# Kernel tuning notes

Hardware: AMD Instinct MI355X
Metric: run time of the kernel (lower is better)

Reference implementation:

```python
import jax, jax.numpy as jnp
import numpy as np

B, C, H, W = 4, 512, 64, 64
WS = 32          # window size (square)
NHEADS = 8
GROUPS = 32      # GroupNorm groups (ldm Normalize)
EPS = 1e-6


def setup_inputs() -> dict:
    key = jax.random.key(0)
    ks = jax.random.split(key, 6)
    p = lambda k: jax.random.normal(k, (C, C), jnp.float32) * 0.02
    return {
        "x": jax.random.normal(ks[0], (B, C, H, W), jnp.float32),
        "norm_scale": jnp.ones((C,), jnp.float32),
        "norm_bias": jnp.zeros((C,), jnp.float32),
        "wq": p(ks[1]), "bq": jnp.zeros((C,), jnp.float32),
        "wk": p(ks[2]), "bk": jnp.zeros((C,), jnp.float32),
        "wv": p(ks[3]), "bv": jnp.zeros((C,), jnp.float32),
        "wo": p(ks[4]), "bo": jnp.zeros((C,), jnp.float32),
    }


def _group_norm(x, scale, bias):
    b, c, h, w = x.shape
    xg = x.reshape(b, GROUPS, c // GROUPS, h, w)
    mu = xg.mean(axis=(2, 3, 4), keepdims=True)
    var = ((xg - mu) ** 2).mean(axis=(2, 3, 4), keepdims=True)
    xn = ((xg - mu) * jax.lax.rsqrt(var + EPS)).reshape(b, c, h, w)
    return xn * scale[None, :, None, None] + bias[None, :, None, None]


def _conv1x1(t, w, b):
    return jnp.einsum('bchw,oc->bohw', t, w) + b[None, :, None, None]


def reference(x, norm_scale, norm_bias, wq, bq, wk, bk, wv, bv, wo, bo):
    b, c, hh, ww = x.shape
    h_ = _group_norm(x, norm_scale, norm_bias)

    # window partition: b c (h w1) (w w2) -> (b h w) c w1 w2  (H,W divisible by WS, no pad)
    nH, nW = hh // WS, ww // WS
    h_ = h_.reshape(b, c, nH, WS, nW, WS).transpose(0, 2, 4, 1, 3, 5)
    h_ = h_.reshape(b * nH * nW, c, WS, WS)

    q = _conv1x1(h_, wq, bq)
    k = _conv1x1(h_, wk, bk)
    v = _conv1x1(h_, wv, bv)

    bw = q.shape[0]
    n = WS * WS
    d = c // NHEADS

    def to_heads(t):  # b c h w -> b heads n d
        t = t.reshape(bw, c, n).transpose(0, 2, 1)          # b n c
        return t.reshape(bw, n, NHEADS, d).transpose(0, 2, 1, 3)

    q, k, v = map(to_heads, (q, k, v))

    scale = 1.0 / jnp.sqrt(jnp.asarray(d, q.dtype))
    scores = jnp.einsum('bhnd,bhmd->bhnm', q, k) * scale    # [bw, heads, n, n]
    attn = jax.nn.softmax(scores, axis=-1)
    out = jnp.einsum('bhnm,bhmd->bhnd', attn, v)
    out = out.transpose(0, 2, 1, 3).reshape(bw, n, c)       # b n c

    # window reverse: (b h w) (w1 w2) c -> b c (h w1) (w w2)
    out = out.reshape(b, nH, nW, WS, WS, c).transpose(0, 5, 1, 3, 2, 4)
    out = out.reshape(b, c, hh, ww)

    out = _conv1x1(out, wo, bo)
    return x + out
```

## Files before the change

### kernel.cpp

```cpp
#include <hip/hip_runtime.h>
#include <math.h>

typedef __bf16 bf16_t;
typedef bf16_t bf16x8 __attribute__((ext_vector_type(8)));
typedef float f32x16 __attribute__((ext_vector_type(16)));
typedef unsigned int u32x4 __attribute__((ext_vector_type(4)));

#define MFMA32(a, b, c) __builtin_amdgcn_mfma_f32_32x32x16_bf16(a, b, c, 0, 0, 0)
#define ROWOF(r, h) (((r) & 3) + 8 * ((r) >> 2) + 4 * (h))


static constexpr size_t OFF_STATS = 0;
static constexpr size_t OFF_W     = 4096;
static constexpr size_t OFF_HT    = OFF_W + 4u * 524288u;
static constexpr size_t OFF_Q     = OFF_HT + 16777216u;
static constexpr size_t OFF_K     = OFF_Q + 16777216u;
static constexpr size_t OFF_V     = OFF_K + 16777216u;
static constexpr size_t OFF_O     = OFF_HT;

__device__ __forceinline__ unsigned short f2bf(float f) {
  unsigned int u = __float_as_uint(f);
  u += 0x7fffu + ((u >> 16) & 1u);
  return (unsigned short)(u >> 16);
}

__global__ __launch_bounds__(256) void wconv_k(const float* __restrict__ w0, const float* __restrict__ w1,
                                               const float* __restrict__ w2, const float* __restrict__ w3,
                                               unsigned short* __restrict__ dst) {
  const float* srcs[4] = {w0, w1, w2, w3};
  const float* src = srcs[blockIdx.y];
  unsigned short* d = dst + (size_t)blockIdx.y * 262144u;
  int i = (blockIdx.x * 256 + threadIdx.x) * 4;
  float4 v = *(const float4*)(src + i);
  unsigned int lo = (unsigned int)f2bf(v.x) | ((unsigned int)f2bf(v.y) << 16);
  unsigned int hi = (unsigned int)f2bf(v.z) | ((unsigned int)f2bf(v.w) << 16);
  uint2 pk; pk.x = lo; pk.y = hi;
  *(uint2*)(d + i) = pk;
}

__global__ __launch_bounds__(256) void gn_stats_k(const float* __restrict__ x, float* __restrict__ stats) {
  int bg = blockIdx.x;
  const float* p = x + (size_t)bg * 65536u;
  int t = threadIdx.x;
  float s = 0.f, ss = 0.f;
  for (int i = t * 4; i < 65536; i += 1024) {
    float4 v = *(const float4*)(p + i);
    s += v.x + v.y + v.z + v.w;
    ss += v.x * v.x + v.y * v.y + v.z * v.z + v.w * v.w;
  }
  for (int m = 1; m <= 32; m <<= 1) { s += __shfl_xor(s, m); ss += __shfl_xor(ss, m); }
  __shared__ float rs[4], rss[4];
  int wv = t >> 6;
  if ((t & 63) == 0) { rs[wv] = s; rss[wv] = ss; }
  __syncthreads();
  if (t == 0) {
    s = rs[0] + rs[1] + rs[2] + rs[3];
    ss = rss[0] + rss[1] + rss[2] + rss[3];
    float mean = s * (1.f / 65536.f);
    float var = ss * (1.f / 65536.f) - mean * mean;
    stats[bg * 2] = mean;
    stats[bg * 2 + 1] = rsqrtf(var + 1e-6f);
  }
}

__global__ __launch_bounds__(256) void gn_apply_k(const float* __restrict__ x, const float* __restrict__ scale,
                                                  const float* __restrict__ bias, const float* __restrict__ stats,
                                                  unsigned short* __restrict__ ht) {
  __shared__ float tile[64][65];
  int blk = blockIdx.x;
  int b = blk >> 9, cblk = (blk >> 6) & 7, sblk = blk & 63;
  int c0 = cblk * 64, s0 = sblk * 64;
  int t = threadIdx.x;
#pragma unroll
  for (int p = 0; p < 4; ++p) {
    int i = p * 16 + (t >> 4);
    int j = (t & 15) * 4;
    int c = c0 + i;
    float mean = stats[(b * 32 + (c >> 4)) * 2];
    float rstd = stats[(b * 32 + (c >> 4)) * 2 + 1];
    float a = rstd * scale[c];
    float b2 = bias[c] - mean * a;
    float4 v = *(const float4*)(x + ((size_t)(b * 512 + c)) * 4096u + s0 + j);
    tile[i][j + 0] = v.x * a + b2;
    tile[i][j + 1] = v.y * a + b2;
    tile[i][j + 2] = v.z * a + b2;
    tile[i][j + 3] = v.w * a + b2;
  }
  __syncthreads();
#pragma unroll
  for (int p = 0; p < 8; ++p) {
    int jj = p * 8 + (t >> 5);
    int c2 = (t & 31) * 2;
    unsigned int pk = (unsigned int)f2bf(tile[c2][jj]) | ((unsigned int)f2bf(tile[c2 + 1][jj]) << 16);
    *(unsigned int*)(ht + ((size_t)b * 4096u + s0 + jj) * 512u + c0 + c2) = pk;
  }
}

__global__ __launch_bounds__(256, 2) void qkv_gemm_k(const unsigned short* __restrict__ wbf,
                                                     const unsigned short* __restrict__ ht,
                                                     const float* __restrict__ bq, const float* __restrict__ bk,
                                                     const float* __restrict__ bv,
                                                     unsigned short* __restrict__ Qatt,
                                                     unsigned short* __restrict__ Katt,
                                                     unsigned short* __restrict__ Vt) {
  int proj = blockIdx.z >> 2, b = blockIdx.z & 3;
  const unsigned short* W = wbf + (size_t)proj * 262144u;
  const float* biasp = (proj == 0) ? bq : (proj == 1) ? bk : bv;
  int o0 = blockIdx.x * 128, s0 = blockIdx.y * 128;
  __shared__ unsigned short Wl[128 * 72];
  __shared__ unsigned short Xl[128 * 72];
  int t = threadIdx.x, lane = t & 63, wv = t >> 6;
  int col_l = lane & 31, half = lane >> 5;
  int qm = (wv >> 1) * 64, qn = (wv & 1) * 64;
  f32x16 acc[2][2];
#pragma unroll
  for (int i = 0; i < 2; i++)
#pragma unroll
    for (int j = 0; j < 2; j++)
#pragma unroll
      for (int r = 0; r < 16; r++) acc[i][j][r] = 0.f;

  const unsigned short* hb = ht + ((size_t)b * 4096u + s0) * 512u;
  for (int kb = 0; kb < 512; kb += 64) {
    __syncthreads();
    {
      int row = t >> 3, ch = (t & 7) * 8;
#pragma unroll
      for (int p = 0; p < 4; ++p, row += 32) {
        *(uint4*)(Wl + row * 72 + ch) = *(const uint4*)(W + (size_t)(o0 + row) * 512u + kb + ch);
        *(uint4*)(Xl + row * 72 + ch) = *(const uint4*)(hb + (size_t)row * 512u + kb + ch);
      }
    }
    __syncthreads();
    const unsigned short* aT = (proj == 2) ? Wl : Xl;
    const unsigned short* bT = (proj == 2) ? Xl : Wl;
#pragma unroll
    for (int ks = 0; ks < 64; ks += 16) {
      bf16x8 a0 = *(const bf16x8*)(aT + (qm + col_l) * 72 + ks + 8 * half);
      bf16x8 a1 = *(const bf16x8*)(aT + (qm + 32 + col_l) * 72 + ks + 8 * half);
      bf16x8 b0 = *(const bf16x8*)(bT + (qn + col_l) * 72 + ks + 8 * half);
      bf16x8 b1 = *(const bf16x8*)(bT + (qn + 32 + col_l) * 72 + ks + 8 * half);
      acc[0][0] = MFMA32(a0, b0, acc[0][0]);
      acc[0][1] = MFMA32(a0, b1, acc[0][1]);
      acc[1][0] = MFMA32(a1, b0, acc[1][0]);
      acc[1][1] = MFMA32(a1, b1, acc[1][1]);
    }
  }

  if (proj <= 1) {
    unsigned short* dst = (proj == 0) ? Qatt : Katt;
#pragma unroll
    for (int i = 0; i < 2; i++)
#pragma unroll
      for (int j = 0; j < 2; j++) {
        int o = o0 + qn + 32 * j + col_l;
        int head = o >> 6, dd = o & 63;
        float bb = biasp[o];
#pragma unroll
        for (int r = 0; r < 16; r++) {
          int s = s0 + qm + 32 * i + ROWOF(r, half);
          int h = s >> 6, w = s & 63;
          int win = b * 4 + (h >> 5) * 2 + (w >> 5);
          int n = ((h & 31) << 5) | (w & 31);
          dst[(((size_t)(win * 8 + head)) * 1024u + n) * 64u + dd] = f2bf(acc[i][j][r] + bb);
        }
      }
  } else {
#pragma unroll
    for (int i = 0; i < 2; i++)
#pragma unroll
      for (int j = 0; j < 2; j++) {
        int s = s0 + qn + 32 * j + col_l;
        int h = s >> 6, w = s & 63;
        int win = b * 4 + (h >> 5) * 2 + (w >> 5);
        int n = ((h & 31) << 5) | (w & 31);
#pragma unroll
        for (int r = 0; r < 16; r++) {
          int o = o0 + qm + 32 * i + ROWOF(r, half);
          int head = o >> 6, dd = o & 63;
          Vt[(((size_t)(win * 8 + head)) * 64u + dd) * 1024u + n] = f2bf(acc[i][j][r] + biasp[o]);
        }
      }
  }
}

__global__ __launch_bounds__(256, 3) void attn_k(const unsigned short* __restrict__ Qatt,
                                                 const unsigned short* __restrict__ Katt,
                                                 const unsigned short* __restrict__ Vt,
                                                 unsigned short* __restrict__ Oimg) {
  int wh_idx = blockIdx.x, rb = blockIdx.y;
  int win = wh_idx >> 3, head = wh_idx & 7;
  int t = threadIdx.x, lane = t & 63, wv = t >> 6;
  int col_l = lane & 31, half = lane >> 5;
  __shared__ unsigned short Kl[128 * 72];
  __shared__ unsigned short Vl[64 * 136];
  const size_t wh = (size_t)wh_idx;
  const unsigned short* Qb = Qatt + wh * 65536u;
  const unsigned short* Kb = Katt + wh * 65536u;
  const unsigned short* Vb = Vt + wh * 65536u;

  int qrow = rb * 128 + wv * 32 + col_l;
  bf16x8 qf[4];
#pragma unroll
  for (int kk = 0; kk < 4; kk++) qf[kk] = *(const bf16x8*)(Qb + (size_t)qrow * 64u + kk * 16 + 8 * half);

  f32x16 oacc[2];
#pragma unroll
  for (int j = 0; j < 2; j++)
#pragma unroll
    for (int r = 0; r < 16; r++) oacc[j][r] = 0.f;
  float lsum = 0.f;

  const float SC = 0.125f * 1.44269504f;

  for (int kt = 0; kt < 8; ++kt) {
    __syncthreads();
    {
      int row = t >> 3, ch = (t & 7) * 8;
#pragma unroll
      for (int p = 0; p < 4; ++p, row += 32)
        *(uint4*)(Kl + row * 72 + ch) = *(const uint4*)(Kb + ((size_t)(kt * 128 + row)) * 64u + ch);
      int vrow = t >> 4, vch = (t & 15) * 8;
#pragma unroll
      for (int p = 0; p < 4; ++p, vrow += 16)
        *(uint4*)(Vl + vrow * 136 + vch) = *(const uint4*)(Vb + (size_t)vrow * 1024u + kt * 128 + vch);
    }
    __syncthreads();

    f32x16 sacc[4];
#pragma unroll
    for (int jb = 0; jb < 4; jb++)
#pragma unroll
      for (int r = 0; r < 16; r++) sacc[jb][r] = 0.f;
#pragma unroll
    for (int jb = 0; jb < 4; jb++) {
#pragma unroll
      for (int kk = 0; kk < 4; kk++) {
        bf16x8 af = *(const bf16x8*)(Kl + (jb * 32 + col_l) * 72 + kk * 16 + 8 * half);
        sacc[jb] = MFMA32(af, qf[kk], sacc[jb]);
      }
    }

#pragma unroll
    for (int jb = 0; jb < 4; jb++) {
      float p[16];
#pragma unroll
      for (int r = 0; r < 16; r++) p[r] = __builtin_amdgcn_exp2f(sacc[jb][r] * SC);
      float ps = ((p[0] + p[1]) + (p[2] + p[3])) + ((p[4] + p[5]) + (p[6] + p[7]));
      ps += ((p[8] + p[9]) + (p[10] + p[11])) + ((p[12] + p[13]) + (p[14] + p[15]));
      lsum += ps;
      unsigned int pk[8];
#pragma unroll
      for (int j = 0; j < 8; j++)
        pk[j] = __builtin_amdgcn_perm(__float_as_uint(p[2 * j + 1]), __float_as_uint(p[2 * j]), 0x07060302u);
      unsigned int rA = __shfl_xor((int)(half ? pk[0] : pk[2]), 32);
      unsigned int rB = __shfl_xor((int)(half ? pk[1] : pk[3]), 32);
      unsigned int rC = __shfl_xor((int)(half ? pk[4] : pk[6]), 32);
      unsigned int rD = __shfl_xor((int)(half ? pk[5] : pk[7]), 32);
      u32x4 f0, f1;
      f0[0] = half ? rA : pk[0];
      f0[1] = half ? rB : pk[1];
      f0[2] = half ? pk[2] : rA;
      f0[3] = half ? pk[3] : rB;
      f1[0] = half ? rC : pk[4];
      f1[1] = half ? rD : pk[5];
      f1[2] = half ? pk[6] : rC;
      f1[3] = half ? pk[7] : rD;
      bf16x8 pa0 = __builtin_bit_cast(bf16x8, f0);
      bf16x8 pa1 = __builtin_bit_cast(bf16x8, f1);
#pragma unroll
      for (int dblk = 0; dblk < 2; dblk++) {
        bf16x8 v0 = *(const bf16x8*)(Vl + (dblk * 32 + col_l) * 136 + (jb * 2 + 0) * 16 + 8 * half);
        bf16x8 v1 = *(const bf16x8*)(Vl + (dblk * 32 + col_l) * 136 + (jb * 2 + 1) * 16 + 8 * half);
        oacc[dblk] = MFMA32(pa0, v0, oacc[dblk]);
        oacc[dblk] = MFMA32(pa1, v1, oacc[dblk]);
      }
    }
  }

  float l = lsum + __shfl_xor(lsum, 32);
  float inv = 1.f / l;

  int b = win >> 2, whn = (win >> 1) & 1, wwn = win & 1;
#pragma unroll
  for (int r = 0; r < 16; r++) {
    int qr = ROWOF(r, half);
    float invr = __shfl(inv, qr);
    int ntok = rb * 128 + wv * 32 + qr;
    int h = whn * 32 + (ntok >> 5), w = wwn * 32 + (ntok & 31);
    int s = h * 64 + w;
    size_t rowbase = ((size_t)b * 4096u + s) * 512u + head * 64;
    Oimg[rowbase + col_l] = f2bf(oacc[0][r] * invr);
    Oimg[rowbase + 32 + col_l] = f2bf(oacc[1][r] * invr);
  }
}

__global__ __launch_bounds__(256, 2) void out_gemm_k(const unsigned short* __restrict__ wo_bf,
                                                     const unsigned short* __restrict__ Oimg,
                                                     const float* __restrict__ bo, const float* __restrict__ x,
                                                     float* __restrict__ out) {
  int b = blockIdx.z;
  int o0 = blockIdx.x * 128, s0 = blockIdx.y * 128;
  __shared__ unsigned short Wl[128 * 72];
  __shared__ unsigned short Xl[128 * 72];
  int t = threadIdx.x, lane = t & 63, wv = t >> 6;
  int col_l = lane & 31, half = lane >> 5;
  int qm = (wv >> 1) * 64, qn = (wv & 1) * 64;
  f32x16 acc[2][2];
#pragma unroll
  for (int i = 0; i < 2; i++)
#pragma unroll
    for (int j = 0; j < 2; j++)
#pragma unroll
      for (int r = 0; r < 16; r++) acc[i][j][r] = 0.f;

  const unsigned short* ob = Oimg + ((size_t)b * 4096u + s0) * 512u;
  for (int kb = 0; kb < 512; kb += 64) {
    __syncthreads();
    {
      int row = t >> 3, ch = (t & 7) * 8;
#pragma unroll
      for (int p = 0; p < 4; ++p, row += 32) {
        *(uint4*)(Wl + row * 72 + ch) = *(const uint4*)(wo_bf + (size_t)(o0 + row) * 512u + kb + ch);
        *(uint4*)(Xl + row * 72 + ch) = *(const uint4*)(ob + (size_t)row * 512u + kb + ch);
      }
    }
    __syncthreads();
#pragma unroll
    for (int ks = 0; ks < 64; ks += 16) {
      bf16x8 a0 = *(const bf16x8*)(Wl + (qm + col_l) * 72 + ks + 8 * half);
      bf16x8 a1 = *(const bf16x8*)(Wl + (qm + 32 + col_l) * 72 + ks + 8 * half);
      bf16x8 b0 = *(const bf16x8*)(Xl + (qn + col_l) * 72 + ks + 8 * half);
      bf16x8 b1 = *(const bf16x8*)(Xl + (qn + 32 + col_l) * 72 + ks + 8 * half);
      acc[0][0] = MFMA32(a0, b0, acc[0][0]);
      acc[0][1] = MFMA32(a0, b1, acc[0][1]);
      acc[1][0] = MFMA32(a1, b0, acc[1][0]);
      acc[1][1] = MFMA32(a1, b1, acc[1][1]);
    }
  }
#pragma unroll
  for (int i = 0; i < 2; i++)
#pragma unroll
    for (int j = 0; j < 2; j++) {
      int s = s0 + qn + 32 * j + col_l;
#pragma unroll
      for (int r = 0; r < 16; r++) {
        int o = o0 + qm + 32 * i + ROWOF(r, half);
        size_t idx = ((size_t)b * 512u + o) * 4096u + s;
        out[idx] = x[idx] + acc[i][j][r] + bo[o];
      }
    }
}

extern "C" void kernel_launch(void* const* d_in, const int* in_sizes, int n_in,
                              void* d_out, int out_size, void* d_ws, size_t ws_size,
                              hipStream_t stream) {
  const float* x = (const float*)d_in[0];
  const float* nsc = (const float*)d_in[1];
  const float* nbi = (const float*)d_in[2];
  const float* wq = (const float*)d_in[3];
  const float* bq = (const float*)d_in[4];
  const float* wk = (const float*)d_in[5];
  const float* bk = (const float*)d_in[6];
  const float* wvp = (const float*)d_in[7];
  const float* bv = (const float*)d_in[8];
  const float* wo = (const float*)d_in[9];
  const float* bo = (const float*)d_in[10];
  float* out = (float*)d_out;
  char* ws = (char*)d_ws;

  float* stats = (float*)(ws + OFF_STATS);
  unsigned short* wbf = (unsigned short*)(ws + OFF_W);
  unsigned short* ht = (unsigned short*)(ws + OFF_HT);
  unsigned short* Qatt = (unsigned short*)(ws + OFF_Q);
  unsigned short* Katt = (unsigned short*)(ws + OFF_K);
  unsigned short* Vt = (unsigned short*)(ws + OFF_V);
  unsigned short* Oimg = (unsigned short*)(ws + OFF_O);

  wconv_k<<<dim3(256, 4), 256, 0, stream>>>(wq, wk, wvp, wo, wbf);
  gn_stats_k<<<128, 256, 0, stream>>>(x, stats);
  gn_apply_k<<<2048, 256, 0, stream>>>(x, nsc, nbi, stats, ht);
  qkv_gemm_k<<<dim3(4, 32, 12), 256, 0, stream>>>(wbf, ht, bq, bk, bv, Qatt, Katt, Vt);
  attn_k<<<dim3(128, 8), 256, 0, stream>>>(Qatt, Katt, Vt, Oimg);
  out_gemm_k<<<dim3(4, 32, 4), 256, 0, stream>>>(wbf + 3u * 262144u, Oimg, bo, x, out);
}
```

Measured before the change: 272.7 us.

## Double-buffer shared-memory tiles with register prefetch in GEMM and attention kernels

Converts the QKV GEMM, attention and output GEMM kernels to a double-buffered LDS scheme. The next K-slice (or K/V tile) is loaded from global memory into registers while the MFMAs run on the current buffer, and one of the two barriers per iteration is dropped. In exchange it doubles LDS use and raises register pressure. The attention kernel's launch-bounds occupancy hint is lowered from 3 to 2 blocks per CU to make room.

Result: slower. 325.1 us (+19.2%).

```diff
diff --git a/kernel.cpp b/kernel.cpp
--- a/kernel.cpp
+++ b/kernel.cpp
@@ -107,8 +107,8 @@
   const unsigned short* W = wbf + (size_t)proj * 262144u;
   const float* biasp = (proj == 0) ? bq : (proj == 1) ? bk : bv;
   int o0 = blockIdx.x * 128, s0 = blockIdx.y * 128;
-  __shared__ unsigned short Wl[128 * 72];
-  __shared__ unsigned short Xl[128 * 72];
+  __shared__ unsigned short Wl[2][128 * 72];
+  __shared__ unsigned short Xl[2][128 * 72];
   int t = threadIdx.x, lane = t & 63, wv = t >> 6;
   int col_l = lane & 31, half = lane >> 5;
   int qm = (wv >> 1) * 64, qn = (wv & 1) * 64;
@@ -121,19 +121,35 @@
       for (int r = 0; r < 16; r++) acc[i][j][r] = 0.f;
 
   const unsigned short* hb = ht + ((size_t)b * 4096u + s0) * 512u;
-  for (int kb = 0; kb < 512; kb += 64) {
+  int row = t >> 3, ch = (t & 7) * 8;
+
+  uint4 wr[4], xr[4];
+#pragma unroll
+  for (int p = 0; p < 4; ++p) {
+    wr[p] = *(const uint4*)(W + (size_t)(o0 + row + 32 * p) * 512u + ch);
+    xr[p] = *(const uint4*)(hb + (size_t)(row + 32 * p) * 512u + ch);
+  }
+
+  for (int kb8 = 0; kb8 < 8; ++kb8) {
+    int buf = kb8 & 1;
+    unsigned short* Wc = Wl[buf];
+    unsigned short* Xc = Xl[buf];
+#pragma unroll
+    for (int p = 0; p < 4; ++p) {
+      *(uint4*)(Wc + (row + 32 * p) * 72 + ch) = wr[p];
+      *(uint4*)(Xc + (row + 32 * p) * 72 + ch) = xr[p];
+    }
     __syncthreads();
-    {
-      int row = t >> 3, ch = (t & 7) * 8;
-#pragma unroll
-      for (int p = 0; p < 4; ++p, row += 32) {
-        *(uint4*)(Wl + row * 72 + ch) = *(const uint4*)(W + (size_t)(o0 + row) * 512u + kb + ch);
-        *(uint4*)(Xl + row * 72 + ch) = *(const uint4*)(hb + (size_t)row * 512u + kb + ch);
-      }
-    }
-    __syncthreads();
-    const unsigned short* aT = (proj == 2) ? Wl : Xl;
-    const unsigned short* bT = (proj == 2) ? Xl : Wl;
+    if (kb8 < 7) {
+      int kb = (kb8 + 1) * 64;
+#pragma unroll
+      for (int p = 0; p < 4; ++p) {
+        wr[p] = *(const uint4*)(W + (size_t)(o0 + row + 32 * p) * 512u + kb + ch);
+        xr[p] = *(const uint4*)(hb + (size_t)(row + 32 * p) * 512u + kb + ch);
+      }
+    }
+    const unsigned short* aT = (proj == 2) ? Wc : Xc;
+    const unsigned short* bT = (proj == 2) ? Xc : Wc;
 #pragma unroll
     for (int ks = 0; ks < 64; ks += 16) {
       bf16x8 a0 = *(const bf16x8*)(aT + (qm + col_l) * 72 + ks + 8 * half);
@@ -184,7 +200,7 @@
   }
 }
 
-__global__ __launch_bounds__(256, 3) void attn_k(const unsigned short* __restrict__ Qatt,
+__global__ __launch_bounds__(256, 2) void attn_k(const unsigned short* __restrict__ Qatt,
                                                  const unsigned short* __restrict__ Katt,
                                                  const unsigned short* __restrict__ Vt,
                                                  unsigned short* __restrict__ Oimg) {
@@ -192,13 +208,23 @@
   int win = wh_idx >> 3, head = wh_idx & 7;
   int t = threadIdx.x, lane = t & 63, wv = t >> 6;
   int col_l = lane & 31, half = lane >> 5;
-  __shared__ unsigned short Kl[128 * 72];
-  __shared__ unsigned short Vl[64 * 136];
+  __shared__ unsigned short Kl[2][128 * 72];
+  __shared__ unsigned short Vl[2][64 * 136];
   const size_t wh = (size_t)wh_idx;
   const unsigned short* Qb = Qatt + wh * 65536u;
   const unsigned short* Kb = Katt + wh * 65536u;
   const unsigned short* Vb = Vt + wh * 65536u;
 
+  int krow = t >> 3, kch = (t & 7) * 8;
+  int vrow = t >> 4, vch = (t & 15) * 8;
+
+  uint4 kr[4], vr[4];
+#pragma unroll
+  for (int p = 0; p < 4; ++p) {
+    kr[p] = *(const uint4*)(Kb + (size_t)(krow + 32 * p) * 64u + kch);
+    vr[p] = *(const uint4*)(Vb + (size_t)(vrow + 16 * p) * 1024u + vch);
+  }
+
   int qrow = rb * 128 + wv * 32 + col_l;
   bf16x8 qf[4];
 #pragma unroll
@@ -214,18 +240,22 @@
   const float SC = 0.125f * 1.44269504f;
 
   for (int kt = 0; kt < 8; ++kt) {
+    unsigned short* Kc = Kl[kt & 1];
+    unsigned short* Vc = Vl[kt & 1];
+#pragma unroll
+    for (int p = 0; p < 4; ++p) {
+      *(uint4*)(Kc + (krow + 32 * p) * 72 + kch) = kr[p];
+      *(uint4*)(Vc + (vrow + 16 * p) * 136 + vch) = vr[p];
+    }
     __syncthreads();
-    {
-      int row = t >> 3, ch = (t & 7) * 8;
-#pragma unroll
-      for (int p = 0; p < 4; ++p, row += 32)
-        *(uint4*)(Kl + row * 72 + ch) = *(const uint4*)(Kb + ((size_t)(kt * 128 + row)) * 64u + ch);
-      int vrow = t >> 4, vch = (t & 15) * 8;
-#pragma unroll
-      for (int p = 0; p < 4; ++p, vrow += 16)
-        *(uint4*)(Vl + vrow * 136 + vch) = *(const uint4*)(Vb + (size_t)vrow * 1024u + kt * 128 + vch);
-    }
-    __syncthreads();
+    if (kt < 7) {
+      int nk = (kt + 1) * 128;
+#pragma unroll
+      for (int p = 0; p < 4; ++p) {
+        kr[p] = *(const uint4*)(Kb + (size_t)(nk + krow + 32 * p) * 64u + kch);
+        vr[p] = *(const uint4*)(Vb + (size_t)(vrow + 16 * p) * 1024u + nk + vch);
+      }
+    }
 
     f32x16 sacc[4];
 #pragma unroll
@@ -236,7 +266,7 @@
     for (int jb = 0; jb < 4; jb++) {
 #pragma unroll
       for (int kk = 0; kk < 4; kk++) {
-        bf16x8 af = *(const bf16x8*)(Kl + (jb * 32 + col_l) * 72 + kk * 16 + 8 * half);
+        bf16x8 af = *(const bf16x8*)(Kc + (jb * 32 + col_l) * 72 + kk * 16 + 8 * half);
         sacc[jb] = MFMA32(af, qf[kk], sacc[jb]);
       }
     }
@@ -270,8 +300,8 @@
       bf16x8 pa1 = __builtin_bit_cast(bf16x8, f1);
 #pragma unroll
       for (int dblk = 0; dblk < 2; dblk++) {
-        bf16x8 v0 = *(const bf16x8*)(Vl + (dblk * 32 + col_l) * 136 + (jb * 2 + 0) * 16 + 8 * half);
-        bf16x8 v1 = *(const bf16x8*)(Vl + (dblk * 32 + col_l) * 136 + (jb * 2 + 1) * 16 + 8 * half);
+        bf16x8 v0 = *(const bf16x8*)(Vc + (dblk * 32 + col_l) * 136 + (jb * 2 + 0) * 16 + 8 * half);
+        bf16x8 v1 = *(const bf16x8*)(Vc + (dblk * 32 + col_l) * 136 + (jb * 2 + 1) * 16 + 8 * half);
         oacc[dblk] = MFMA32(pa0, v0, oacc[dblk]);
         oacc[dblk] = MFMA32(pa1, v1, oacc[dblk]);
       }
@@ -301,8 +331,8 @@
                                                      float* __restrict__ out) {
   int b = blockIdx.z;
   int o0 = blockIdx.x * 128, s0 = blockIdx.y * 128;
-  __shared__ unsigned short Wl[128 * 72];
-  __shared__ unsigned short Xl[128 * 72];
+  __shared__ unsigned short Wl[2][128 * 72];
+  __shared__ unsigned short Xl[2][128 * 72];
   int t = threadIdx.x, lane = t & 63, wv = t >> 6;
   int col_l = lane & 31, half = lane >> 5;
   int qm = (wv >> 1) * 64, qn = (wv & 1) * 64;
@@ -315,23 +345,39 @@
       for (int r = 0; r < 16; r++) acc[i][j][r] = 0.f;
 
   const unsigned short* ob = Oimg + ((size_t)b * 4096u + s0) * 512u;
-  for (int kb = 0; kb < 512; kb += 64) {
+  int row = t >> 3, ch = (t & 7) * 8;
+
+  uint4 wr[4], xr[4];
+#pragma unroll
+  for (int p = 0; p < 4; ++p) {
+    wr[p] = *(const uint4*)(wo_bf + (size_t)(o0 + row + 32 * p) * 512u + ch);
+    xr[p] = *(const uint4*)(ob + (size_t)(row + 32 * p) * 512u + ch);
+  }
+
+  for (int kb8 = 0; kb8 < 8; ++kb8) {
+    int buf = kb8 & 1;
+    unsigned short* Wc = Wl[buf];
+    unsigned short* Xc = Xl[buf];
+#pragma unroll
+    for (int p = 0; p < 4; ++p) {
+      *(uint4*)(Wc + (row + 32 * p) * 72 + ch) = wr[p];
+      *(uint4*)(Xc + (row + 32 * p) * 72 + ch) = xr[p];
+    }
     __syncthreads();
-    {
-      int row = t >> 3, ch = (t & 7) * 8;
-#pragma unroll
-      for (int p = 0; p < 4; ++p, row += 32) {
-        *(uint4*)(Wl + row * 72 + ch) = *(const uint4*)(wo_bf + (size_t)(o0 + row) * 512u + kb + ch);
-        *(uint4*)(Xl + row * 72 + ch) = *(const uint4*)(ob + (size_t)row * 512u + kb + ch);
-      }
-    }
-    __syncthreads();
+    if (kb8 < 7) {
+      int kb = (kb8 + 1) * 64;
+#pragma unroll
+      for (int p = 0; p < 4; ++p) {
+        wr[p] = *(const uint4*)(wo_bf + (size_t)(o0 + row + 32 * p) * 512u + kb + ch);
+        xr[p] = *(const uint4*)(ob + (size_t)(row + 32 * p) * 512u + kb + ch);
+      }
+    }
 #pragma unroll
     for (int ks = 0; ks < 64; ks += 16) {
-      bf16x8 a0 = *(const bf16x8*)(Wl + (qm + col_l) * 72 + ks + 8 * half);
-      bf16x8 a1 = *(const bf16x8*)(Wl + (qm + 32 + col_l) * 72 + ks + 8 * half);
-      bf16x8 b0 = *(const bf16x8*)(Xl + (qn + col_l) * 72 + ks + 8 * half);
-      bf16x8 b1 = *(const bf16x8*)(Xl + (qn + 32 + col_l) * 72 + ks + 8 * half);
+      bf16x8 a0 = *(const bf16x8*)(Wc + (qm + col_l) * 72 + ks + 8 * half);
+      bf16x8 a1 = *(const bf16x8*)(Wc + (qm + 32 + col_l) * 72 + ks + 8 * half);
+      bf16x8 b0 = *(const bf16x8*)(Xc + (qn + col_l) * 72 + ks + 8 * half);
+      bf16x8 b1 = *(const bf16x8*)(Xc + (qn + 32 + col_l) * 72 + ks + 8 * half);
       acc[0][0] = MFMA32(a0, b0, acc[0][0]);
       acc[0][1] = MFMA32(a0, b1, acc[0][1]);
       acc[1][0] = MFMA32(a1, b0, acc[1][0]);
```

## Double-buffer attention K/V tiles with async global-to-LDS loads and XOR swizzle

Applied to the files above, without the earlier changes.

Replaces the synchronous register-staged K/V tile loads in the attention kernel with direct global_load_lds transfers into two LDS buffers, prefetching tile kt+1 while tile kt is computed. The padded LDS layout becomes an XOR-swizzled layout that avoids bank conflicts without padding. LDS use doubles, so occupancy hint drops from 3 to 2 blocks per CU. The waitcnt and single barrier per iteration must correctly order the async writes against reads of the other buffer.

Result: no change. 271.5 us (-0.4%).

```diff
diff --git a/kernel.cpp b/kernel.cpp
--- a/kernel.cpp
+++ b/kernel.cpp
@@ -22,6 +22,13 @@
   unsigned int u = __float_as_uint(f);
   u += 0x7fffu + ((u >> 16) & 1u);
   return (unsigned short)(u >> 16);
+}
+
+__device__ __forceinline__ void gl_lds16(const unsigned short* g, unsigned short* lds_base) {
+  __builtin_amdgcn_global_load_lds(
+      (const __attribute__((address_space(1))) unsigned int*)g,
+      (__attribute__((address_space(3))) unsigned int*)(unsigned int)(unsigned long long)lds_base,
+      16, 0, 0);
 }
 
 __global__ __launch_bounds__(256) void wconv_k(const float* __restrict__ w0, const float* __restrict__ w1,
@@ -184,7 +191,7 @@
   }
 }
 
-__global__ __launch_bounds__(256, 3) void attn_k(const unsigned short* __restrict__ Qatt,
+__global__ __launch_bounds__(256, 2) void attn_k(const unsigned short* __restrict__ Qatt,
                                                  const unsigned short* __restrict__ Katt,
                                                  const unsigned short* __restrict__ Vt,
                                                  unsigned short* __restrict__ Oimg) {
@@ -192,13 +199,29 @@
   int win = wh_idx >> 3, head = wh_idx & 7;
   int t = threadIdx.x, lane = t & 63, wv = t >> 6;
   int col_l = lane & 31, half = lane >> 5;
-  __shared__ unsigned short Kl[128 * 72];
-  __shared__ unsigned short Vl[64 * 136];
+  __shared__ unsigned short Kl[2][128 * 64];
+  __shared__ unsigned short Vl[2][64 * 128];
   const size_t wh = (size_t)wh_idx;
   const unsigned short* Qb = Qatt + wh * 65536u;
   const unsigned short* Kb = Katt + wh * 65536u;
   const unsigned short* Vb = Vt + wh * 65536u;
 
+  int ks_r[4], ks_off[4], vs_r[4], vs_off[4];
+#pragma unroll
+  for (int i = 0; i < 4; ++i) {
+    int s = wv * 256 + i * 64 + lane;
+    ks_r[i] = s >> 3;
+    ks_off[i] = ((s & 7) ^ (ks_r[i] & 7)) * 8;
+    vs_r[i] = s >> 4;
+    vs_off[i] = ((s & 15) ^ (vs_r[i] & 15)) * 8;
+  }
+
+#pragma unroll
+  for (int i = 0; i < 4; ++i) {
+    gl_lds16(Kb + (size_t)ks_r[i] * 64u + ks_off[i], &Kl[0][0] + wv * 2048 + i * 512);
+    gl_lds16(Vb + (size_t)vs_r[i] * 1024u + vs_off[i], &Vl[0][0] + wv * 2048 + i * 512);
+  }
+
   int qrow = rb * 128 + wv * 32 + col_l;
   bf16x8 qf[4];
 #pragma unroll
@@ -212,20 +235,24 @@
   float lsum = 0.f;
 
   const float SC = 0.125f * 1.44269504f;
+  const int kx = col_l & 7;
+  const int vx = col_l & 15;
 
   for (int kt = 0; kt < 8; ++kt) {
+    const unsigned short* Kc = Kl[kt & 1];
+    const unsigned short* Vc = Vl[kt & 1];
+    __builtin_amdgcn_s_waitcnt(0x0F70);
     __syncthreads();
-    {
-      int row = t >> 3, ch = (t & 7) * 8;
-#pragma unroll
-      for (int p = 0; p < 4; ++p, row += 32)
-        *(uint4*)(Kl + row * 72 + ch) = *(const uint4*)(Kb + ((size_t)(kt * 128 + row)) * 64u + ch);
-      int vrow = t >> 4, vch = (t & 15) * 8;
-#pragma unroll
-      for (int p = 0; p < 4; ++p, vrow += 16)
-        *(uint4*)(Vl + vrow * 136 + vch) = *(const uint4*)(Vb + (size_t)vrow * 1024u + kt * 128 + vch);
-    }
-    __syncthreads();
+    if (kt < 7) {
+      unsigned short* Kn = &Kl[(kt + 1) & 1][0];
+      unsigned short* Vn = &Vl[(kt + 1) & 1][0];
+      int nk = (kt + 1) * 128;
+#pragma unroll
+      for (int i = 0; i < 4; ++i) {
+        gl_lds16(Kb + (size_t)(nk + ks_r[i]) * 64u + ks_off[i], Kn + wv * 2048 + i * 512);
+        gl_lds16(Vb + (size_t)vs_r[i] * 1024u + nk + vs_off[i], Vn + wv * 2048 + i * 512);
+      }
+    }
 
     f32x16 sacc[4];
 #pragma unroll
@@ -234,9 +261,10 @@
       for (int r = 0; r < 16; r++) sacc[jb][r] = 0.f;
 #pragma unroll
     for (int jb = 0; jb < 4; jb++) {
+      const unsigned short* Krow = Kc + (jb * 32 + col_l) * 64;
 #pragma unroll
       for (int kk = 0; kk < 4; kk++) {
-        bf16x8 af = *(const bf16x8*)(Kl + (jb * 32 + col_l) * 72 + kk * 16 + 8 * half);
+        bf16x8 af = *(const bf16x8*)(Krow + (((kk * 2 + half) ^ kx) * 8));
         sacc[jb] = MFMA32(af, qf[kk], sacc[jb]);
       }
     }
@@ -270,8 +298,9 @@
       bf16x8 pa1 = __builtin_bit_cast(bf16x8, f1);
 #pragma unroll
       for (int dblk = 0; dblk < 2; dblk++) {
-        bf16x8 v0 = *(const bf16x8*)(Vl + (dblk * 32 + col_l) * 136 + (jb * 2 + 0) * 16 + 8 * half);
-        bf16x8 v1 = *(const bf16x8*)(Vl + (dblk * 32 + col_l) * 136 + (jb * 2 + 1) * 16 + 8 * half);
+        const unsigned short* Vrow = Vc + (dblk * 32 + col_l) * 128;
+        bf16x8 v0 = *(const bf16x8*)(Vrow + (((jb * 4 + half) ^ vx) * 8));
+        bf16x8 v1 = *(const bf16x8*)(Vrow + (((jb * 4 + 2 + half) ^ vx) * 8));
         oacc[dblk] = MFMA32(pa0, v0, oacc[dblk]);
         oacc[dblk] = MFMA32(pa1, v1, oacc[dblk]);
       }
```

## Double-buffer K/V tiles via async global-to-LDS loads with XOR swizzle

Applied to the files above, without the earlier changes.

The attention kernel now stages K and V through two 64-key LDS buffers filled with global_load_lds, so the next tile loads while the current one is computed. Padded layouts are replaced by an XOR-swizzled 64-wide layout to avoid bank conflicts. The softmax scale is folded into Q at projection time, and the occupancy hint is raised from 3 to 4 blocks. Risks are more barriers per key (half-size tiles) and the correctness of the waitcnt encoding and swizzle math.

Result: faster. 263.5 us (-3.4%).

```diff
diff --git a/kernel.cpp b/kernel.cpp
--- a/kernel.cpp
+++ b/kernel.cpp
@@ -18,10 +18,19 @@
 static constexpr size_t OFF_V     = OFF_K + 16777216u;
 static constexpr size_t OFF_O     = OFF_HT;
 
+static constexpr float QSC = 0.125f * 1.44269504f;
+
 __device__ __forceinline__ unsigned short f2bf(float f) {
   unsigned int u = __float_as_uint(f);
   u += 0x7fffu + ((u >> 16) & 1u);
   return (unsigned short)(u >> 16);
+}
+
+__device__ __forceinline__ void gl_lds16(const unsigned short* g, unsigned short* lds_base) {
+  __builtin_amdgcn_global_load_lds(
+      (const __attribute__((address_space(1))) unsigned int*)g,
+      (__attribute__((address_space(3))) unsigned int*)(unsigned int)(unsigned long long)lds_base,
+      16, 0, 0);
 }
 
 __global__ __launch_bounds__(256) void wconv_k(const float* __restrict__ w0, const float* __restrict__ w1,
@@ -149,6 +158,7 @@
 
   if (proj <= 1) {
     unsigned short* dst = (proj == 0) ? Qatt : Katt;
+    float osc = (proj == 0) ? QSC : 1.0f;
 #pragma unroll
     for (int i = 0; i < 2; i++)
 #pragma unroll
@@ -162,7 +172,7 @@
           int h = s >> 6, w = s & 63;
           int win = b * 4 + (h >> 5) * 2 + (w >> 5);
           int n = ((h & 31) << 5) | (w & 31);
-          dst[(((size_t)(win * 8 + head)) * 1024u + n) * 64u + dd] = f2bf(acc[i][j][r] + bb);
+          dst[(((size_t)(win * 8 + head)) * 1024u + n) * 64u + dd] = f2bf((acc[i][j][r] + bb) * osc);
         }
       }
   } else {
@@ -184,7 +194,7 @@
   }
 }
 
-__global__ __launch_bounds__(256, 3) void attn_k(const unsigned short* __restrict__ Qatt,
+__global__ __launch_bounds__(256, 4) void attn_k(const unsigned short* __restrict__ Qatt,
                                                  const unsigned short* __restrict__ Katt,
                                                  const unsigned short* __restrict__ Vt,
                                                  unsigned short* __restrict__ Oimg) {
@@ -192,13 +202,24 @@
   int win = wh_idx >> 3, head = wh_idx & 7;
   int t = threadIdx.x, lane = t & 63, wv = t >> 6;
   int col_l = lane & 31, half = lane >> 5;
-  __shared__ unsigned short Kl[128 * 72];
-  __shared__ unsigned short Vl[64 * 136];
+  __shared__ unsigned short Kl[2][64 * 64];
+  __shared__ unsigned short Vl[2][64 * 64];
   const size_t wh = (size_t)wh_idx;
   const unsigned short* Qb = Qatt + wh * 65536u;
   const unsigned short* Kb = Katt + wh * 65536u;
   const unsigned short* Vb = Vt + wh * 65536u;
 
+  int sl0 = wv * 128 + lane, sl1 = sl0 + 64;
+  int r0 = sl0 >> 3, off0 = ((sl0 & 7) ^ (r0 & 7)) * 8;
+  int r1 = sl1 >> 3, off1 = ((sl1 & 7) ^ (r1 & 7)) * 8;
+  unsigned short* Kd0 = &Kl[0][0] + wv * 1024;
+  unsigned short* Vd0 = &Vl[0][0] + wv * 1024;
+
+  gl_lds16(Kb + (size_t)r0 * 64u + off0, Kd0);
+  gl_lds16(Kb + (size_t)r1 * 64u + off1, Kd0 + 512);
+  gl_lds16(Vb + (size_t)r0 * 1024u + off0, Vd0);
+  gl_lds16(Vb + (size_t)r1 * 1024u + off1, Vd0 + 512);
+
   int qrow = rb * 128 + wv * 32 + col_l;
   bf16x8 qf[4];
 #pragma unroll
@@ -211,41 +232,43 @@
     for (int r = 0; r < 16; r++) oacc[j][r] = 0.f;
   float lsum = 0.f;
 
-  const float SC = 0.125f * 1.44269504f;
-
-  for (int kt = 0; kt < 8; ++kt) {
+  const int kx = col_l & 7;
+
+  for (int kt = 0; kt < 16; ++kt) {
+    const unsigned short* Kc = Kl[kt & 1];
+    const unsigned short* Vc = Vl[kt & 1];
+    __builtin_amdgcn_s_waitcnt(0x0F70);
     __syncthreads();
-    {
-      int row = t >> 3, ch = (t & 7) * 8;
-#pragma unroll
-      for (int p = 0; p < 4; ++p, row += 32)
-        *(uint4*)(Kl + row * 72 + ch) = *(const uint4*)(Kb + ((size_t)(kt * 128 + row)) * 64u + ch);
-      int vrow = t >> 4, vch = (t & 15) * 8;
-#pragma unroll
-      for (int p = 0; p < 4; ++p, vrow += 16)
-        *(uint4*)(Vl + vrow * 136 + vch) = *(const uint4*)(Vb + (size_t)vrow * 1024u + kt * 128 + vch);
-    }
-    __syncthreads();
-
-    f32x16 sacc[4];
-#pragma unroll
-    for (int jb = 0; jb < 4; jb++)
+    if (kt < 15) {
+      unsigned short* Kn = &Kl[(kt + 1) & 1][0] + wv * 1024;
+      unsigned short* Vn = &Vl[(kt + 1) & 1][0] + wv * 1024;
+      int nk = (kt + 1) * 64;
+      gl_lds16(Kb + (size_t)(nk + r0) * 64u + off0, Kn);
+      gl_lds16(Kb + (size_t)(nk + r1) * 64u + off1, Kn + 512);
+      gl_lds16(Vb + (size_t)r0 * 1024u + nk + off0, Vn);
+      gl_lds16(Vb + (size_t)r1 * 1024u + nk + off1, Vn + 512);
+    }
+
+    f32x16 sacc[2];
+#pragma unroll
+    for (int jb = 0; jb < 2; jb++)
 #pragma unroll
       for (int r = 0; r < 16; r++) sacc[jb][r] = 0.f;
 #pragma unroll
-    for (int jb = 0; jb < 4; jb++) {
+    for (int jb = 0; jb < 2; jb++) {
+      const unsigned short* Krow = Kc + (jb * 32 + col_l) * 64;
 #pragma unroll
       for (int kk = 0; kk < 4; kk++) {
-        bf16x8 af = *(const bf16x8*)(Kl + (jb * 32 + col_l) * 72 + kk * 16 + 8 * half);
+        bf16x8 af = *(const bf16x8*)(Krow + (((kk * 2 + half) ^ kx) * 8));
         sacc[jb] = MFMA32(af, qf[kk], sacc[jb]);
       }
     }
 
 #pragma unroll
-    for (int jb = 0; jb < 4; jb++) {
+    for (int jb = 0; jb < 2; jb++) {
       float p[16];
 #pragma unroll
-      for (int r = 0; r < 16; r++) p[r] = __builtin_amdgcn_exp2f(sacc[jb][r] * SC);
+      for (int r = 0; r < 16; r++) p[r] = __builtin_amdgcn_exp2f(sacc[jb][r]);
       float ps = ((p[0] + p[1]) + (p[2] + p[3])) + ((p[4] + p[5]) + (p[6] + p[7]));
       ps += ((p[8] + p[9]) + (p[10] + p[11])) + ((p[12] + p[13]) + (p[14] + p[15]));
       lsum += ps;
@@ -270,8 +293,9 @@
       bf16x8 pa1 = __builtin_bit_cast(bf16x8, f1);
 #pragma unroll
       for (int dblk = 0; dblk < 2; dblk++) {
-        bf16x8 v0 = *(const bf16x8*)(Vl + (dblk * 32 + col_l) * 136 + (jb * 2 + 0) * 16 + 8 * half);
-        bf16x8 v1 = *(const bf16x8*)(Vl + (dblk * 32 + col_l) * 136 + (jb * 2 + 1) * 16 + 8 * half);
+        const unsigned short* Vrow = Vc + (dblk * 32 + col_l) * 64;
+        bf16x8 v0 = *(const bf16x8*)(Vrow + (((jb * 4 + half) ^ kx) * 8));
+        bf16x8 v1 = *(const bf16x8*)(Vrow + (((jb * 4 + 2 + half) ^ kx) * 8));
         oacc[dblk] = MFMA32(pa0, v0, oacc[dblk]);
         oacc[dblk] = MFMA32(pa1, v1, oacc[dblk]);
       }
```
